# Performance work log

Hardware: AMD Instinct MI355X
Metric: run time of the kernel (lower is better)

## Reference

```python
import jax, jax.numpy as jnp
import numpy as np

B, T, I, H = 8192, 658, 7, 1
D1, D2, D3 = 1024, 512, 128


def setup_inputs() -> dict:
    key = jax.random.key(0)
    ks = jax.random.split(key, 14)
    return {
        "x": jax.random.normal(ks[0], (B, T, I), dtype=jnp.float32),
        "h0": jax.random.uniform(ks[1], (1, B, H), dtype=jnp.float32),
        "W_ih": jax.random.normal(ks[2], (H, I), dtype=jnp.float32) * 0.3,
        "W_hh": jax.random.normal(ks[3], (H, H), dtype=jnp.float32) * 0.3,
        "b_ih": jax.random.normal(ks[4], (H,), dtype=jnp.float32) * 0.1,
        "b_hh": jax.random.normal(ks[5], (H,), dtype=jnp.float32) * 0.1,
        "w1": jax.random.normal(ks[6], (D1, T), dtype=jnp.float32) * 0.03,
        "b1": jax.random.normal(ks[7], (D1,), dtype=jnp.float32) * 0.01,
        "w2": jax.random.normal(ks[8], (D2, D1), dtype=jnp.float32) * 0.03,
        "b2": jax.random.normal(ks[9], (D2,), dtype=jnp.float32) * 0.01,
        "w3": jax.random.normal(ks[10], (D3, D2), dtype=jnp.float32) * 0.03,
        "b3": jax.random.normal(ks[11], (D3,), dtype=jnp.float32) * 0.01,
        "w4": jax.random.normal(ks[12], (T, D3), dtype=jnp.float32) * 0.03,
        "b4": jax.random.normal(ks[13], (T,), dtype=jnp.float32) * 0.01,
    }


def _forward(x, h0, W_ih, W_hh, b_ih, b_hh, w1, b1, w2, b2, w3, b3, w4, b4):
    # Precompute input projection for all timesteps: [T, B, H]
    xw = jnp.einsum("bti,hi->tbh", x, W_ih) + b_ih

    def step(h, xw_t):  # h: [B, H]
        h_new = jnp.tanh(xw_t + h @ W_hh.T + b_hh)
        return h_new, h_new

    h_last, hs = jax.lax.scan(step, h0[0], xw)  # hs: [T, B, H]
    out = jnp.transpose(hs, (1, 0, 2)).reshape(-1, T)  # [B, T] (view(-1, seq))

    out = jax.nn.relu(out @ w1.T + b1)
    out = jax.nn.relu(out @ w2.T + b2)
    out = jax.nn.relu(out @ w3.T + b3)
    out = out @ w4.T + b4
    return out, h_last[None]  # hidden: [1, B, H]


def reference(x, h0, W_ih, W_hh, b_ih, b_hh, w1, b1, w2, b2, w3, b3, w4, b4):
    return _forward(x, h0, W_ih, W_hh, b_ih, b_hh, w1, b1, w2, b2, w3, b3, w4, b4)
```

## Files before the change

### kernel.cpp

```cpp
#include <hip/hip_runtime.h>
#include <hip/hip_bf16.h>
#include <stdint.h>
#include <stddef.h>

#define B_  8192
#define T_  658
#define I_  7
#define TP  672
#define D1_ 1024
#define D2_ 512
#define D3_ 128
#define NP4 768

#define NB2 32
#define CT  32
#define NCH 21
#define SCANBLKS 256
#define SCTHR 320

#define CVTOT (D1_*TP + D2_*D1_ + D3_*D2_ + NP4*D3_)
#define CVBLKS ((CVTOT + SCTHR - 1) / SCTHR)

typedef __bf16 bf16x8 __attribute__((ext_vector_type(8)));
typedef float  floatx4 __attribute__((ext_vector_type(4)));

__device__ __forceinline__ void gload_lds16(const void* g, void* l) {
    __builtin_amdgcn_global_load_lds(
        (const __attribute__((address_space(1))) void*)g,
        (__attribute__((address_space(3))) void*)l, 16, 0, 0);
}

__device__ __forceinline__ unsigned int pack_bf16x2(float a, float b) {
    unsigned int ua = __float_as_uint(a);
    unsigned int ub = __float_as_uint(b);
    ua += 0x7fffu + ((ua >> 16) & 1u);
    ub += 0x7fffu + ((ub >> 16) & 1u);
    return (ua >> 16) | (ub & 0xffff0000u);
}

__device__ __forceinline__ void load_unit(const float* __restrict__ gp, int tb,
                                          float* __restrict__ xr) {
    if (tb <= T_ - 4) {
#pragma unroll
        for (int k = 0; k < 14; ++k) {
            const float2 f = *(const float2*)(gp + 2 * k);
            xr[2 * k]     = f.x;
            xr[2 * k + 1] = f.y;
        }
    } else {
        const int nfl = (T_ - tb) * I_;
#pragma unroll
        for (int k = 0; k < 28; ++k)
            xr[k] = (k < nfl) ? gp[k] : 0.0f;
    }
}

__global__ __launch_bounds__(SCTHR) void scan_conv_kernel(
    const float* __restrict__ x, const float* __restrict__ h0,
    const float* __restrict__ Wih, const float* __restrict__ Whh,
    const float* __restrict__ bih, const float* __restrict__ bhh,
    __bf16* __restrict__ A0, float* __restrict__ hlast,
    const float* __restrict__ w1, const float* __restrict__ w2,
    const float* __restrict__ w3, const float* __restrict__ w4,
    __bf16* __restrict__ w1b, __bf16* __restrict__ w2b,
    __bf16* __restrict__ w3b, __bf16* __restrict__ w4b) {
    if (blockIdx.x >= SCANBLKS) {
        int i = (blockIdx.x - SCANBLKS) * SCTHR + threadIdx.x;
        if (i < D1_ * TP) {
            int r = i / TP, c = i - r * TP;
            w1b[i] = (__bf16)(c < T_ ? w1[r * T_ + c] : 0.0f);
            return;
        }
        i -= D1_ * TP;
        if (i < D2_ * D1_) { w2b[i] = (__bf16)w2[i]; return; }
        i -= D2_ * D1_;
        if (i < D3_ * D2_) { w3b[i] = (__bf16)w3[i]; return; }
        i -= D3_ * D2_;
        if (i < NP4 * D3_) {
            int r = i / D3_, c = i - r * D3_;
            w4b[i] = (__bf16)(r < T_ ? w4[r * D3_ + c] : 0.0f);
        }
        return;
    }

    __shared__ float        lds_x[2][CT][NB2 + 1];
    __shared__ unsigned int lds_o[2][NB2 * 17];

    const int tid = threadIdx.x;
    const int b0 = blockIdx.x * NB2;

    const float whh = Whh[0], bh = bhh[0], bi = bih[0];
    float wih[I_];
#pragma unroll
    for (int j = 0; j < I_; ++j) wih[j] = Wih[j];

    const float C2L = 2.8853900817779268f;
    const float whhc = whh * C2L;
    const float m2w = -2.0f * whhc;

    float h = 0.0f, r = 0.0f;
    if (tid < NB2) {
        h = h0[b0 + tid];
        r = (1.0f - h) * 0.5f;
    }
    unsigned int res[CT / 2];

    const int unit = tid - 64;
    const int prow = unit >> 3, pu = unit & 7;
    const float* gpu = x + (size_t)(b0 + prow) * (T_ * I_) + (size_t)(pu * 4) * I_;
    float xr[28];
    if (tid >= 64) load_unit(gpu, pu * 4, xr);

    for (int it = 0; it < NCH + 2; ++it) {
        if (tid >= 64 && it < NCH) {
#pragma unroll
            for (int n = 0; n < 4; ++n) {
                float s = bi;
#pragma unroll
                for (int i = 0; i < I_; ++i)
                    s = fmaf(xr[n * 7 + i], wih[i], s);
                lds_x[it & 1][pu * 4 + n][prow] = s;
            }
            if (it + 1 < NCH)
                load_unit(gpu + (size_t)(it + 1) * (CT * I_),
                          (it + 1) * CT + pu * 4, xr);
        }
        if (tid < NB2 && it >= 1 && it <= NCH) {
            const int ck = it - 1;
            const float* lx = &lds_x[ck & 1][0][tid];
            if (ck < NCH - 1) {
#pragma unroll
                for (int k = 0; k < CT; k += 2) {
                    float xv0 = lx[k * (NB2 + 1)];
                    float xv1 = lx[(k + 1) * (NB2 + 1)];
                    float c0 = fmaf(xv0 + bh, C2L, whhc);
                    float c1 = fmaf(xv1 + bh, C2L, whhc);
                    r = __builtin_amdgcn_rcpf(__builtin_amdgcn_exp2f(fmaf(m2w, r, c0)) + 1.0f);
                    float h0v = fmaf(-2.0f, r, 1.0f);
                    r = __builtin_amdgcn_rcpf(__builtin_amdgcn_exp2f(fmaf(m2w, r, c1)) + 1.0f);
                    h = fmaf(-2.0f, r, 1.0f);
                    res[k >> 1] = pack_bf16x2(h0v, h);
                }
            } else {
                const int nval = T_ - ck * CT;
#pragma unroll
                for (int k = 0; k < CT; k += 2) {
                    float r0 = 0.0f, r1 = 0.0f;
                    if (k < nval) {
                        float xv0 = lx[k * (NB2 + 1)];
                        r = __builtin_amdgcn_rcpf(
                            __builtin_amdgcn_exp2f(fmaf(m2w, r, fmaf(xv0 + bh, C2L, whhc))) + 1.0f);
                        h = fmaf(-2.0f, r, 1.0f);
                        r0 = h;
                    }
                    if (k + 1 < nval) {
                        float xv1 = lx[(k + 1) * (NB2 + 1)];
                        r = __builtin_amdgcn_rcpf(
                            __builtin_amdgcn_exp2f(fmaf(m2w, r, fmaf(xv1 + bh, C2L, whhc))) + 1.0f);
                        h = fmaf(-2.0f, r, 1.0f);
                        r1 = h;
                    }
                    res[k >> 1] = pack_bf16x2(r0, r1);
                }
            }
#pragma unroll
            for (int j = 0; j < 16; ++j) lds_o[ck & 1][tid * 17 + j] = res[j];
        }
        if (it >= 2 && tid < 128) {
            const int ck = it - 2;
            const int bl = tid >> 2, q = tid & 3;
            uint4 v;
            v.x = lds_o[ck & 1][bl * 17 + q * 4 + 0];
            v.y = lds_o[ck & 1][bl * 17 + q * 4 + 1];
            v.z = lds_o[ck & 1][bl * 17 + q * 4 + 2];
            v.w = lds_o[ck & 1][bl * 17 + q * 4 + 3];
            *(uint4*)(A0 + (size_t)(b0 + bl) * TP + ck * CT + q * 8) = v;
        }
        __syncthreads();
    }
    if (tid < NB2) hlast[b0 + tid] = h;
}

template<int BM, int BN, int MINW>
__global__ __launch_bounds__(256, MINW) void gemm_bt(
    const __bf16* __restrict__ A, const __bf16* __restrict__ W,
    const float* __restrict__ bias, __bf16* __restrict__ outb,
    float* __restrict__ outf, int K, int Npad, int Nreal, int relu) {
    constexpr int MI = BM / 32;
    constexpr int NJ = BN / 32;
    constexpr int nA = BM / 64;
    constexpr int nB = BN / 64;
    __shared__ __align__(16) __bf16 As[BM * 32];
    __shared__ __align__(16) __bf16 Bs[BN * 32];

    const int tid = threadIdx.x;
    int mb, nb;
    {
        const int nbx = gridDim.x;
        const int bid = blockIdx.y * nbx + blockIdx.x;
        if ((nbx & 7) == 0) {
            const int mpx = nbx >> 3;
            const int xcd = bid & 7, j = bid >> 3;
            mb = xcd * mpx + (j % mpx);
            nb = j / mpx;
        } else {
            mb = blockIdx.x; nb = blockIdx.y;
        }
    }
    const int m0 = mb * BM, n0 = nb * BN;
    const int lane = tid & 63, wave = tid >> 6;
    const int wm = (wave & 1) * (BM / 2), wn = (wave >> 1) * (BN / 2);
    const int quad = lane >> 4, l16 = lane & 15;

    const int eoff = tid * 8;
    const int rowS = eoff >> 5;
    const int colS = eoff & 31;
    const __bf16* gaa[nA];
    const __bf16* gbb[nB];
    __bf16* laa[nA];
    __bf16* lbb[nB];
#pragma unroll
    for (int c = 0; c < nA; ++c) {
        gaa[c] = A + (size_t)(m0 + rowS + c * 64) * K + colS;
        laa[c] = As + c * 2048 + (tid & 192) * 8;
    }
#pragma unroll
    for (int c = 0; c < nB; ++c) {
        gbb[c] = W + (size_t)(n0 + rowS + c * 64) * K + colS;
        lbb[c] = Bs + c * 2048 + (tid & 192) * 8;
    }

    floatx4 acc[MI][NJ] = {};

    for (int k0 = 0; k0 < K; k0 += 32) {
#pragma unroll
        for (int c = 0; c < nA; ++c) gload_lds16(gaa[c] + k0, laa[c]);
#pragma unroll
        for (int c = 0; c < nB; ++c) gload_lds16(gbb[c] + k0, lbb[c]);
        __syncthreads();

        bf16x8 af[MI], bg[NJ];
#pragma unroll
        for (int i = 0; i < MI; ++i)
            af[i] = *(const bf16x8*)(As + (wm + i * 16 + l16) * 32 + quad * 8);
#pragma unroll
        for (int j = 0; j < NJ; ++j)
            bg[j] = *(const bf16x8*)(Bs + (wn + j * 16 + l16) * 32 + quad * 8);
#pragma unroll
        for (int i = 0; i < MI; ++i)
#pragma unroll
            for (int j = 0; j < NJ; ++j)
                acc[i][j] = __builtin_amdgcn_mfma_f32_16x16x32_bf16(af[i], bg[j], acc[i][j], 0, 0, 0);
        __syncthreads();
    }

#pragma unroll
    for (int j = 0; j < NJ; ++j) {
        const int n = n0 + wn + j * 16 + l16;
        const float bv = (n < Nreal) ? bias[n] : 0.0f;
#pragma unroll
        for (int i = 0; i < MI; ++i) {
#pragma unroll
            for (int r = 0; r < 4; ++r) {
                const int m = m0 + wm + i * 16 + quad * 4 + r;
                float v = acc[i][j][r] + bv;
                if (relu) v = fmaxf(v, 0.0f);
                if (outb) {
                    outb[(size_t)m * Npad + n] = (__bf16)v;
                } else if (n < Nreal) {
                    outf[(size_t)m * Nreal + n] = v;
                }
            }
        }
    }
}

extern "C" void kernel_launch(void* const* d_in, const int* in_sizes, int n_in,
                              void* d_out, int out_size, void* d_ws, size_t ws_size,
                              hipStream_t stream) {
    const float* x   = (const float*)d_in[0];
    const float* h0  = (const float*)d_in[1];
    const float* Wih = (const float*)d_in[2];
    const float* Whh = (const float*)d_in[3];
    const float* bih = (const float*)d_in[4];
    const float* bhh = (const float*)d_in[5];
    const float* w1  = (const float*)d_in[6];
    const float* b1  = (const float*)d_in[7];
    const float* w2  = (const float*)d_in[8];
    const float* b2  = (const float*)d_in[9];
    const float* w3  = (const float*)d_in[10];
    const float* b3  = (const float*)d_in[11];
    const float* w4  = (const float*)d_in[12];
    const float* b4  = (const float*)d_in[13];
    float* out = (float*)d_out;
    char* ws = (char*)d_ws;

    __bf16* w1b = (__bf16*)(ws + 0);
    __bf16* w2b = (__bf16*)(ws + 1376256);
    __bf16* w3b = (__bf16*)(ws + 2424832);
    __bf16* w4b = (__bf16*)(ws + 2555904);
    __bf16* A0  = (__bf16*)(ws + 2752512);
    __bf16* A1  = (__bf16*)(ws + 13762560);
    __bf16* A2  = (__bf16*)(ws + 30539776);
    __bf16* A3  = (__bf16*)(ws + 38928384);

    scan_conv_kernel<<<SCANBLKS + CVBLKS, SCTHR, 0, stream>>>(
        x, h0, Wih, Whh, bih, bhh, A0, out + (size_t)B_ * T_,
        w1, w2, w3, w4, w1b, w2b, w3b, w4b);

    gemm_bt<128,128,2><<<dim3(64, 8), 256, 0, stream>>>(A0, w1b, b1, A1, nullptr, TP,  D1_, D1_, 1);
    gemm_bt<128,64,2> <<<dim3(64, 8), 256, 0, stream>>>(A1, w2b, b2, A2, nullptr, D1_, D2_, D2_, 1);
    gemm_bt<64,64,4>  <<<dim3(128, 2), 256, 0, stream>>>(A2, w3b, b3, A3, nullptr, D2_, D3_, D3_, 1);
    gemm_bt<64,128,4> <<<dim3(128, 6), 256, 0, stream>>>(A3, w4b, b4, nullptr, out, D3_, NP4, T_, 0);
}
```

Before: 315.4 us.

## Stage x chunks into LDS via async global_load_lds with double buffering

Replaces the per-thread register loads of x in the scan kernel with asynchronous global-to-LDS 16-byte loads into a double-buffered raw LDS staging area. The loads are issued one chunk ahead and gated with explicit vmcnt waits, and the input projection then reads from LDS. The weight-conversion blocks become a fixed-size grid-stride loop, and __syncthreads is replaced by an explicit lgkmcnt wait plus s_barrier. This aims to hide global load latency for the serial scan, at the cost of a much larger LDS footprint (64KB extra) that may reduce occupancy.

After: 322.4 us. +2.2%, slower.

```diff
diff --git a/kernel.cpp b/kernel.cpp
--- a/kernel.cpp
+++ b/kernel.cpp
@@ -19,7 +19,7 @@
 #define SCTHR 320
 
 #define CVTOT (D1_*TP + D2_*D1_ + D3_*D2_ + NP4*D3_)
-#define CVBLKS ((CVTOT + SCTHR - 1) / SCTHR)
+#define CVBLKS 512
 
 typedef __bf16 bf16x8 __attribute__((ext_vector_type(8)));
 typedef float  floatx4 __attribute__((ext_vector_type(4)));
@@ -38,21 +38,16 @@
     return (ua >> 16) | (ub & 0xffff0000u);
 }
 
-__device__ __forceinline__ void load_unit(const float* __restrict__ gp, int tb,
-                                          float* __restrict__ xr) {
-    if (tb <= T_ - 4) {
-#pragma unroll
-        for (int k = 0; k < 14; ++k) {
-            const float2 f = *(const float2*)(gp + 2 * k);
-            xr[2 * k]     = f.x;
-            xr[2 * k + 1] = f.y;
-        }
-    } else {
-        const int nfl = (T_ - tb) * I_;
-#pragma unroll
-        for (int k = 0; k < 28; ++k)
-            xr[k] = (k < nfl) ? gp[k] : 0.0f;
-    }
+template<int S>
+__device__ __forceinline__ void stage_chunk(const float* __restrict__ x,
+                                            float* lbuf, int b0, int pw, int l, int c) {
+    const int srow = 8 * pw + (l >> 3);
+    const float* sbase = x + (size_t)(b0 + srow) * (T_ * I_) - 2 * (srow & 1)
+                         + (size_t)c * (CT * I_) + 4 * (l & 7);
+    float* ldst = lbuf + pw * 2048;
+#pragma unroll
+    for (int s = 0; s < S; ++s)
+        gload_lds16(sbase + 32 * s, ldst + s * 256);
 }
 
 __global__ __launch_bounds__(SCTHR) void scan_conv_kernel(
@@ -65,24 +60,29 @@
     __bf16* __restrict__ w1b, __bf16* __restrict__ w2b,
     __bf16* __restrict__ w3b, __bf16* __restrict__ w4b) {
     if (blockIdx.x >= SCANBLKS) {
-        int i = (blockIdx.x - SCANBLKS) * SCTHR + threadIdx.x;
-        if (i < D1_ * TP) {
-            int r = i / TP, c = i - r * TP;
-            w1b[i] = (__bf16)(c < T_ ? w1[r * T_ + c] : 0.0f);
-            return;
-        }
-        i -= D1_ * TP;
-        if (i < D2_ * D1_) { w2b[i] = (__bf16)w2[i]; return; }
-        i -= D2_ * D1_;
-        if (i < D3_ * D2_) { w3b[i] = (__bf16)w3[i]; return; }
-        i -= D3_ * D2_;
-        if (i < NP4 * D3_) {
-            int r = i / D3_, c = i - r * D3_;
-            w4b[i] = (__bf16)(r < T_ ? w4[r * D3_ + c] : 0.0f);
+        const int stride = CVBLKS * SCTHR;
+        for (int i0 = (blockIdx.x - SCANBLKS) * SCTHR + threadIdx.x; i0 < CVTOT;
+             i0 += stride) {
+            int i = i0;
+            if (i < D1_ * TP) {
+                int r = i / TP, c = i - r * TP;
+                w1b[i] = (__bf16)(c < T_ ? w1[r * T_ + c] : 0.0f);
+                continue;
+            }
+            i -= D1_ * TP;
+            if (i < D2_ * D1_) { w2b[i] = (__bf16)w2[i]; continue; }
+            i -= D2_ * D1_;
+            if (i < D3_ * D2_) { w3b[i] = (__bf16)w3[i]; continue; }
+            i -= D3_ * D2_;
+            {
+                int r = i / D3_, c = i - r * D3_;
+                w4b[i] = (__bf16)(r < T_ ? w4[r * D3_ + c] : 0.0f);
+            }
         }
         return;
     }
 
+    __shared__ __align__(16) float lds_raw[2][8192];
     __shared__ float        lds_x[2][CT][NB2 + 1];
     __shared__ unsigned int lds_o[2][NB2 * 17];
 
@@ -105,25 +105,41 @@
     }
     unsigned int res[CT / 2];
 
-    const int unit = tid - 64;
-    const int prow = unit >> 3, pu = unit & 7;
-    const float* gpu = x + (size_t)(b0 + prow) * (T_ * I_) + (size_t)(pu * 4) * I_;
-    float xr[28];
-    if (tid >= 64) load_unit(gpu, pu * 4, xr);
+    const int pw = (tid >> 6) - 1;
+    const int pl = tid & 63;
+
+    if (tid >= 64) stage_chunk<8>(x, &lds_raw[0][0], b0, pw, pl, 0);
 
     for (int it = 0; it < NCH + 2; ++it) {
         if (tid >= 64 && it < NCH) {
+            if (it + 1 <= NCH - 2) {
+                stage_chunk<8>(x, &lds_raw[(it + 1) & 1][0], b0, pw, pl, it + 1);
+                asm volatile("s_waitcnt vmcnt(8)" ::: "memory");
+            } else if (it + 1 == NCH - 1) {
+                stage_chunk<4>(x, &lds_raw[(it + 1) & 1][0], b0, pw, pl, it + 1);
+                asm volatile("s_waitcnt vmcnt(4)" ::: "memory");
+            } else {
+                asm volatile("s_waitcnt vmcnt(0)" ::: "memory");
+            }
+            const int p = tid - 64;
+            const int prow = p >> 3, pu = p & 7;
+            const float* rbuf = &lds_raw[it & 1][(prow >> 3) * 2048 + (prow & 7) * 32];
+            const int par2 = 2 * (prow & 1);
+            const int tmax = (it == NCH - 1) ? (T_ - it * CT) : CT;
 #pragma unroll
             for (int n = 0; n < 4; ++n) {
-                float s = bi;
-#pragma unroll
-                for (int i = 0; i < I_; ++i)
-                    s = fmaf(xr[n * 7 + i], wih[i], s);
-                lds_x[it & 1][pu * 4 + n][prow] = s;
-            }
-            if (it + 1 < NCH)
-                load_unit(gpu + (size_t)(it + 1) * (CT * I_),
-                          (it + 1) * CT + pu * 4, xr);
+                const int tt = pu * 4 + n;
+                if (tt < tmax) {
+                    const int F0 = tt * 7 + par2;
+                    float s = bi;
+#pragma unroll
+                    for (int i = 0; i < I_; ++i) {
+                        const int F = F0 + i;
+                        s = fmaf(rbuf[(F >> 5) * 256 + (F & 31)], wih[i], s);
+                    }
+                    lds_x[it & 1][tt][prow] = s;
+                }
+            }
         }
         if (tid < NB2 && it >= 1 && it <= NCH) {
             const int ck = it - 1;
@@ -176,7 +192,9 @@
             v.w = lds_o[ck & 1][bl * 17 + q * 4 + 3];
             *(uint4*)(A0 + (size_t)(b0 + bl) * TP + ck * CT + q * 8) = v;
         }
-        __syncthreads();
+        asm volatile("s_waitcnt lgkmcnt(0)" ::: "memory");
+        __builtin_amdgcn_s_barrier();
+        asm volatile("" ::: "memory");
     }
     if (tid < NB2) hlast[b0 + tid] = h;
 }
```

## Double-buffer LDS tiles in GEMM to overlap global loads with MFMA

Applied to the files above, without the earlier changes.

The GEMM kernel now keeps two LDS buffers per operand and prefetches the next K-tile with global_load_lds while MFMAs run on the current one. It replaces the paired __syncthreads with explicit vmcnt waits and raw barriers. The smaller GEMMs' launch-bounds minimum waves drops from 4 to 2 to fit the doubled LDS. The aim is to hide global memory latency, at the cost of more LDS and possibly lower occupancy.

After: 315.5 us. About the same (+0.0%).

```diff
diff --git a/kernel.cpp b/kernel.cpp
--- a/kernel.cpp
+++ b/kernel.cpp
@@ -28,6 +28,14 @@
     __builtin_amdgcn_global_load_lds(
         (const __attribute__((address_space(1))) void*)g,
         (__attribute__((address_space(3))) void*)l, 16, 0, 0);
+}
+
+template<int N> __device__ __forceinline__ void waitcnt_vm() {
+    if constexpr (N == 0)      asm volatile("s_waitcnt vmcnt(0)" ::: "memory");
+    else if constexpr (N == 2) asm volatile("s_waitcnt vmcnt(2)" ::: "memory");
+    else if constexpr (N == 3) asm volatile("s_waitcnt vmcnt(3)" ::: "memory");
+    else if constexpr (N == 4) asm volatile("s_waitcnt vmcnt(4)" ::: "memory");
+    else                       asm volatile("s_waitcnt vmcnt(0)" ::: "memory");
 }
 
 __device__ __forceinline__ unsigned int pack_bf16x2(float a, float b) {
@@ -190,8 +198,9 @@
     constexpr int NJ = BN / 32;
     constexpr int nA = BM / 64;
     constexpr int nB = BN / 64;
-    __shared__ __align__(16) __bf16 As[BM * 32];
-    __shared__ __align__(16) __bf16 Bs[BN * 32];
+    constexpr int LPT = nA + nB;
+    __shared__ __align__(16) __bf16 As[2 * BM * 32];
+    __shared__ __align__(16) __bf16 Bs[2 * BN * 32];
 
     const int tid = threadIdx.x;
     int mb, nb;
@@ -217,41 +226,57 @@
     const int colS = eoff & 31;
     const __bf16* gaa[nA];
     const __bf16* gbb[nB];
-    __bf16* laa[nA];
-    __bf16* lbb[nB];
-#pragma unroll
-    for (int c = 0; c < nA; ++c) {
+#pragma unroll
+    for (int c = 0; c < nA; ++c)
         gaa[c] = A + (size_t)(m0 + rowS + c * 64) * K + colS;
-        laa[c] = As + c * 2048 + (tid & 192) * 8;
-    }
-#pragma unroll
-    for (int c = 0; c < nB; ++c) {
+#pragma unroll
+    for (int c = 0; c < nB; ++c)
         gbb[c] = W + (size_t)(n0 + rowS + c * 64) * K + colS;
-        lbb[c] = Bs + c * 2048 + (tid & 192) * 8;
-    }
+    __bf16* laaB = As + (tid & 192) * 8;
+    __bf16* lbbB = Bs + (tid & 192) * 8;
+
+    auto stage = [&](int t, int cu) {
+        const int k0 = t * 32;
+#pragma unroll
+        for (int c = 0; c < nA; ++c)
+            gload_lds16(gaa[c] + k0, laaB + cu * (BM * 32) + c * 2048);
+#pragma unroll
+        for (int c = 0; c < nB; ++c)
+            gload_lds16(gbb[c] + k0, lbbB + cu * (BN * 32) + c * 2048);
+    };
 
     floatx4 acc[MI][NJ] = {};
 
-    for (int k0 = 0; k0 < K; k0 += 32) {
-#pragma unroll
-        for (int c = 0; c < nA; ++c) gload_lds16(gaa[c] + k0, laa[c]);
-#pragma unroll
-        for (int c = 0; c < nB; ++c) gload_lds16(gbb[c] + k0, lbb[c]);
-        __syncthreads();
+    stage(0, 0);
+    int cur = 0;
+    const int NT = K / 32;
+    for (int t = 0; t < NT; ++t) {
+        if (t + 1 < NT) {
+            stage(t + 1, cur ^ 1);
+            waitcnt_vm<LPT>();
+        } else {
+            waitcnt_vm<0>();
+        }
+        __builtin_amdgcn_s_barrier();
+        asm volatile("" ::: "memory");
 
         bf16x8 af[MI], bg[NJ];
 #pragma unroll
         for (int i = 0; i < MI; ++i)
-            af[i] = *(const bf16x8*)(As + (wm + i * 16 + l16) * 32 + quad * 8);
+            af[i] = *(const bf16x8*)(As + cur * (BM * 32) + (wm + i * 16 + l16) * 32 + quad * 8);
 #pragma unroll
         for (int j = 0; j < NJ; ++j)
-            bg[j] = *(const bf16x8*)(Bs + (wn + j * 16 + l16) * 32 + quad * 8);
+            bg[j] = *(const bf16x8*)(Bs + cur * (BN * 32) + (wn + j * 16 + l16) * 32 + quad * 8);
 #pragma unroll
         for (int i = 0; i < MI; ++i)
 #pragma unroll
             for (int j = 0; j < NJ; ++j)
                 acc[i][j] = __builtin_amdgcn_mfma_f32_16x16x32_bf16(af[i], bg[j], acc[i][j], 0, 0, 0);
-        __syncthreads();
+
+        asm volatile("s_waitcnt lgkmcnt(0)" ::: "memory");
+        __builtin_amdgcn_sched_barrier(0);
+        __builtin_amdgcn_s_barrier();
+        cur ^= 1;
     }
 
 #pragma unroll
@@ -310,6 +335,6 @@
 
     gemm_bt<128,128,2><<<dim3(64, 8), 256, 0, stream>>>(A0, w1b, b1, A1, nullptr, TP,  D1_, D1_, 1);
     gemm_bt<128,64,2> <<<dim3(64, 8), 256, 0, stream>>>(A1, w2b, b2, A2, nullptr, D1_, D2_, D2_, 1);
-    gemm_bt<64,64,4>  <<<dim3(128, 2), 256, 0, stream>>>(A2, w3b, b3, A3, nullptr, D2_, D3_, D3_, 1);
-    gemm_bt<64,128,4> <<<dim3(128, 6), 256, 0, stream>>>(A3, w4b, b4, nullptr, out, D3_, NP4, T_, 0);
-}
+    gemm_bt<64,64,2>  <<<dim3(128, 2), 256, 0, stream>>>(A2, w3b, b3, A3, nullptr, D2_, D3_, D3_, 1);
+    gemm_bt<64,128,2> <<<dim3(128, 6), 256, 0, stream>>>(A3, w4b, b4, nullptr, out, D3_, NP4, T_, 0);
+}
```
